# Optimization experiments

Measured on AMD Instinct MI355X. Metric: run time of the kernel, lower is better.

The kernel has to match this reference:

```python
import jax, jax.numpy as jnp
import numpy as np

S, D = 4096, 2048  # seq_len, embedding_space == qkv_dim


def setup_inputs() -> dict:
    key = jax.random.key(0)
    k1, k2, k3, k4, k5 = jax.random.split(key, 5)
    return {
        "input_embedding": jax.random.normal(k1, (S, D), dtype=jnp.float32),
        "query_embedding": jax.random.normal(k2, (S, D), dtype=jnp.float32),
        "Wq": jax.random.normal(k3, (D, D), dtype=jnp.float32) * 0.02,
        "Wk": jax.random.normal(k4, (D, D), dtype=jnp.float32) * 0.02,
        "Wv": jax.random.normal(k5, (D, D), dtype=jnp.float32) * 0.02,
        "include_mask": 0,  # False -> causal mask applied (module's inverted logic)
    }


def reference(input_embedding, query_embedding, Wq, Wk, Wv, include_mask):
    q = query_embedding @ Wq          # [S, D]
    k = input_embedding @ Wk          # [S, D]
    v = input_embedding @ Wv          # [S, D]
    scores = (q @ k.T) / 10.0         # [S, S]; module hardcodes /10, not sqrt(d)
    if not include_mask:
        # causal: -inf strictly above the diagonal (triu with offset 1)
        s = scores.shape[0]
        causal = jnp.tril(jnp.ones((s, s), dtype=bool))
        scores = jnp.where(causal, scores, -jnp.inf)
    probs = jax.nn.softmax(scores, axis=-1)
    return probs @ v                  # [S, D]
```

## Files before the change

kernel.cpp:

```cpp
#include <hip/hip_runtime.h>
#include <hip/hip_bf16.h>
#include <math.h>

typedef __bf16 bf16_t;
typedef __bf16 bf16x8 __attribute__((ext_vector_type(8)));
typedef float f32x4 __attribute__((ext_vector_type(4)));

enum { EP_BF16 = 0, EP_SCORES = 1, EP_F32 = 2, EP_F32A = 3 };

#define MEMFENCE asm volatile("" ::: "memory")
#define BARRIER() do { MEMFENCE; __builtin_amdgcn_s_barrier(); MEMFENCE; } while (0)

__device__ __forceinline__ void gload_lds16(const void* g, void* l) {
  __builtin_amdgcn_global_load_lds(
      (const __attribute__((address_space(1))) void*)g,
      (__attribute__((address_space(3))) void*)l, 16, 0, 0);
}

template <int N>
__device__ __forceinline__ void wait_vmcnt() {
  if constexpr (N == 0)       asm volatile("s_waitcnt vmcnt(0)" ::: "memory");
  else if constexpr (N == 6)  asm volatile("s_waitcnt vmcnt(6)" ::: "memory");
  else if constexpr (N == 8)  asm volatile("s_waitcnt vmcnt(8)" ::: "memory");
  else if constexpr (N == 12) asm volatile("s_waitcnt vmcnt(12)" ::: "memory");
  else if constexpr (N == 16) asm volatile("s_waitcnt vmcnt(16)" ::: "memory");
  else static_assert(N == 0, "unsupported vmcnt");
}

__device__ __forceinline__ int xcd_swz(int bid, int nwg) {
  const int q = nwg >> 3;
  return (bid & 7) * q + (bid >> 3);
}


template <int TM, bool STG, int WAITN>
__device__ __forceinline__ void do_tile(char* smem, int slot, int sslot, size_t stoff,
                                        const char* const* gbase, const int* lbase,
                                        const int* aoff, const int* boff,
                                        f32x4 (&acc)[TM][4]) {
  bf16x8 bfr[4], af[4];
  if constexpr (TM == 8) {
#pragma unroll
    for (int n = 0; n < 4; ++n) bfr[n] = *(const bf16x8*)(smem + slot + boff[n]);
#pragma unroll
    for (int m = 0; m < 4; ++m) af[m] = *(const bf16x8*)(smem + slot + aoff[m]);
    if constexpr (STG) {
      gload_lds16(gbase[0] + stoff, smem + sslot + lbase[0]);
      gload_lds16(gbase[1] + stoff, smem + sslot + lbase[1]);
    }
    BARRIER();
    asm volatile("s_waitcnt lgkmcnt(0)" ::: "memory");
    __builtin_amdgcn_sched_barrier(0);
    __builtin_amdgcn_s_setprio(1);
#pragma unroll
    for (int m = 0; m < 4; ++m)
#pragma unroll
      for (int n = 0; n < 4; ++n)
        acc[m][n] = __builtin_amdgcn_mfma_f32_16x16x32_bf16(af[m], bfr[n], acc[m][n], 0, 0, 0);
    __builtin_amdgcn_s_setprio(0);
    BARRIER();
#pragma unroll
    for (int m = 0; m < 4; ++m) af[m] = *(const bf16x8*)(smem + slot + aoff[4 + m]);
    if constexpr (STG) {
      gload_lds16(gbase[2] + stoff, smem + sslot + lbase[2]);
      gload_lds16(gbase[3] + stoff, smem + sslot + lbase[3]);
      wait_vmcnt<WAITN>();
    }
    BARRIER();
    asm volatile("s_waitcnt lgkmcnt(0)" ::: "memory");
    __builtin_amdgcn_sched_barrier(0);
    __builtin_amdgcn_s_setprio(1);
#pragma unroll
    for (int m = 0; m < 4; ++m)
#pragma unroll
      for (int n = 0; n < 4; ++n)
        acc[4 + m][n] = __builtin_amdgcn_mfma_f32_16x16x32_bf16(af[m], bfr[n], acc[4 + m][n], 0, 0, 0);
    __builtin_amdgcn_s_setprio(0);
    BARRIER();
  } else {
#pragma unroll
    for (int n = 0; n < 4; ++n) bfr[n] = *(const bf16x8*)(smem + slot + boff[n]);
#pragma unroll
    for (int m = 0; m < 4; ++m) af[m] = *(const bf16x8*)(smem + slot + aoff[m]);
    if constexpr (STG) {
      gload_lds16(gbase[0] + stoff, smem + sslot + lbase[0]);
      gload_lds16(gbase[1] + stoff, smem + sslot + lbase[1]);
      gload_lds16(gbase[2] + stoff, smem + sslot + lbase[2]);
      wait_vmcnt<WAITN>();
    }
    BARRIER();
    asm volatile("s_waitcnt lgkmcnt(0)" ::: "memory");
    __builtin_amdgcn_sched_barrier(0);
    __builtin_amdgcn_s_setprio(1);
#pragma unroll
    for (int m = 0; m < 4; ++m)
#pragma unroll
      for (int n = 0; n < 4; ++n)
        acc[m][n] = __builtin_amdgcn_mfma_f32_16x16x32_bf16(af[m], bfr[n], acc[m][n], 0, 0, 0);
    __builtin_amdgcn_s_setprio(0);
    BARRIER();
  }
}

template <int TM, int EPI, int NSLOT>
__device__ __forceinline__ void gemm_core(
    const bf16_t* __restrict__ A, const bf16_t* __restrict__ B,
    void* __restrict__ Cout, int Nout, int kstride, int klen,
    int row0, int col0, bool causal, float scale, char* smem)
{
  constexpr int BM = TM * 32;
  constexpr int LPT_A = BM / 128;
  constexpr int LPT = LPT_A + 2;
  constexpr int ABYTES = BM * 64;
  constexpr int SLOT = (BM + 256) * 64;
  constexpr int DEPTH = NSLOT - 1;
  constexpr int WAITN = (DEPTH - 1) * LPT;

  const int tid = threadIdx.x;
  const int w = tid >> 6, lane = tid & 63;
  const int wr = w >> 2, wc = w & 3;

  const int nt = klen >> 5;

  const char* gbase[LPT];
  int lbase[LPT];
  {
    const int sd = (tid & 3) ^ ((tid >> 3) & 3);
    const int rrow = tid >> 2;
#pragma unroll
    for (int r = 0; r < LPT; ++r) {
      const bool isA = (r < LPT_A);
      const int rr = isA ? r : (r - LPT_A);
      const int grow = (isA ? row0 : col0) + rr * 128 + rrow;
      const bf16_t* op = isA ? A : B;
      gbase[r] = (const char*)(op + (size_t)grow * kstride) + sd * 16;
      lbase[r] = (isA ? 0 : ABYTES) + rr * 8192 + w * 1024;
    }
  }

  const int fl = lane & 15;
  const int arow_off = fl * 64 + (((lane >> 4) ^ ((fl >> 1) & 3)) * 16);
  int aoff[TM], boff[4];
#pragma unroll
  for (int m = 0; m < TM; ++m) aoff[m] = (wr * (TM * 16) + m * 16) * 64 + arow_off;
#pragma unroll
  for (int n = 0; n < 4; ++n) boff[n] = ABYTES + (wc * 64 + n * 16) * 64 + arow_off;

  f32x4 acc[TM][4] = {};

  const int npro = nt < DEPTH ? nt : DEPTH;
  for (int t = 0; t < npro; ++t)
#pragma unroll
    for (int r = 0; r < LPT; ++r)
      gload_lds16(gbase[r] + (size_t)t * 64, smem + (t % NSLOT) * SLOT + lbase[r]);

  const int nmain = nt - DEPTH;
  if (nmain > 0) {
    wait_vmcnt<WAITN>();
    BARRIER();
    for (int t = 0; t < nmain; ++t)
      do_tile<TM, true, WAITN>(smem, (t % NSLOT) * SLOT, ((t + DEPTH) % NSLOT) * SLOT,
                               (size_t)(t + DEPTH) * 64, gbase, lbase, aoff, boff, acc);
  }

  wait_vmcnt<0>();
  BARRIER();
  for (int t = nmain > 0 ? nmain : 0; t < nt; ++t)
    do_tile<TM, false, 0>(smem, (t % NSLOT) * SLOT, 0, 0, gbase, lbase, aoff, boff, acc);

  const int cr = (lane >> 4) * 4;
  const int cc = lane & 15;
#pragma unroll
  for (int m = 0; m < TM; ++m) {
#pragma unroll
    for (int n = 0; n < 4; ++n) {
#pragma unroll
      for (int i = 0; i < 4; ++i) {
        const int r = row0 + wr * (TM * 16) + m * 16 + cr + i;
        const int c = col0 + wc * 64 + n * 16 + cc;
        float v = acc[m][n][i];
        if (EPI == EP_BF16) {
          ((bf16_t*)Cout)[(size_t)r * Nout + c] = (bf16_t)v;
        } else if (EPI == EP_SCORES) {
          v *= scale;
          if (causal && c > r) v = -INFINITY;
          ((float*)Cout)[(size_t)r * Nout + c] = v;
        } else if (EPI == EP_F32) {
          ((float*)Cout)[(size_t)r * Nout + c] = v;
        } else {
          atomicAdd((float*)Cout + (size_t)r * Nout + c, v);
        }
      }
    }
  }
}

__launch_bounds__(512, 2)
__global__ void qk_k(const bf16_t* __restrict__ qe16, const bf16_t* __restrict__ ie16,
                     const bf16_t* __restrict__ WqT, const bf16_t* __restrict__ WkT,
                     bf16_t* __restrict__ q16, bf16_t* __restrict__ k16) {
  extern __shared__ __align__(16) char smem[];
  int wg = xcd_swz(blockIdx.x, gridDim.x);
  const bf16_t *A, *B; bf16_t* C;
  if (wg < 128) { A = qe16; B = WqT; C = q16; }
  else          { A = ie16; B = WkT; C = k16; wg -= 128; }
  const int row0 = (wg >> 3) * 256, col0 = (wg & 7) * 256;
  gemm_core<8, EP_BF16, 4>(A, B, C, 2048, 2048, 2048, row0, col0, false, 1.f, smem);
}

__launch_bounds__(512, 2)
__global__ void vs_k(const bf16_t* __restrict__ WvT, const bf16_t* __restrict__ ie16,
                     const bf16_t* __restrict__ q16, const bf16_t* __restrict__ k16,
                     bf16_t* __restrict__ vT16, float* __restrict__ scores,
                     const int* __restrict__ maskflag) {
  extern __shared__ __align__(16) char smem[];
  const bool causal = maskflag[0] == 0;
  const int nsc = causal ? 136 : 256;
  const int bid = blockIdx.x;
  if (bid < nsc) {
    const int sid = xcd_swz(bid, nsc);
    int r, c;
    if (causal) {
      r = (int)((sqrtf(8.f * (float)sid + 1.f) - 1.f) * 0.5f);
      while ((r + 1) * (r + 2) / 2 <= sid) ++r;
      while (r * (r + 1) / 2 > sid) --r;
      c = sid - r * (r + 1) / 2;
    } else {
      r = sid >> 4; c = sid & 15;
    }
    gemm_core<8, EP_SCORES, 4>(q16, k16, scores, 4096, 2048, 2048,
                               r * 256, c * 256, causal, 0.1f, smem);
  } else {
    const int j = bid - nsc;
    gemm_core<4, EP_BF16, 6>(WvT, ie16, vT16, 4096, 2048, 2048,
                             (j >> 4) * 128, (j & 15) * 256, false, 1.f, smem);
  }
}

__launch_bounds__(512, 2)
__global__ void smv_k(const bf16_t* __restrict__ WvT, const bf16_t* __restrict__ ie16,
                      bf16_t* __restrict__ vT16,
                      const float* __restrict__ scores, bf16_t* __restrict__ probs,
                      const int* __restrict__ maskflag) {
  extern __shared__ __align__(16) char smem[];
  const bool causal = maskflag[0] == 0;
  const int nv = causal ? 136 : 256;
  const int vbase = causal ? 120 : 0;
  const int bid = blockIdx.x;
  if (bid < nv) {
    const int j = vbase + bid;
    gemm_core<4, EP_BF16, 6>(WvT, ie16, vT16, 4096, 2048, 2048,
                             (j >> 4) * 128, (j & 15) * 256, false, 1.f, smem);
    return;
  }
  const int p = bid - nv;
  if (p >= 2048) return;
  const int tid = threadIdx.x;
  const int h = tid >> 8;
  const int t = tid & 255;
  const int row = 2 * p + h;
  const int L = causal ? (row + 1) : 4096;
  const float* srow = scores + (size_t)row * 4096;
  float v[16];
  float m = -INFINITY;
#pragma unroll
  for (int j = 0; j < 16; ++j) {
    const int idx = t + j * 256;
    v[j] = (idx < L) ? srow[idx] : -INFINITY;
    m = fmaxf(m, v[j]);
  }
#pragma unroll
  for (int off = 32; off >= 1; off >>= 1) m = fmaxf(m, __shfl_xor(m, off));
  __shared__ float redm[8];
  __shared__ float reds[8];
  if ((tid & 63) == 0) redm[tid >> 6] = m;
  __syncthreads();
  m = fmaxf(fmaxf(redm[4 * h + 0], redm[4 * h + 1]),
            fmaxf(redm[4 * h + 2], redm[4 * h + 3]));
  float s = 0.f;
#pragma unroll
  for (int j = 0; j < 16; ++j) {
    v[j] = __expf(v[j] - m);
    s += v[j];
  }
#pragma unroll
  for (int off = 32; off >= 1; off >>= 1) s += __shfl_xor(s, off);
  if ((tid & 63) == 0) reds[tid >> 6] = s;
  __syncthreads();
  s = reds[4 * h + 0] + reds[4 * h + 1] + reds[4 * h + 2] + reds[4 * h + 3];
  const float inv = 1.f / s;
  bf16_t* prow = probs + (size_t)row * 4096;
#pragma unroll
  for (int j = 0; j < 16; ++j) prow[t + j * 256] = (bf16_t)(v[j] * inv);
}

__launch_bounds__(512, 2)
__global__ void pv_k(const bf16_t* __restrict__ probs, const bf16_t* __restrict__ vT16,
                     float* __restrict__ out, const int* __restrict__ maskflag) {
  extern __shared__ __align__(16) char smem[];
  const bool causal = maskflag[0] == 0;
  const int bid = blockIdx.x;
  if (causal) {
    if (bid >= 256) return;
    const int sid  = xcd_swz(bid, 256);
    const int half = sid & 1;
    const int pair = (sid >> 1) & 15;
    const int col  = sid >> 5;
    const int blo = pair, bhi = 31 - pair;
    const int Klo = 128 * (blo + 1);
    const int cut = 2112 - Klo;
    if (half == 0) {
      gemm_core<4, EP_F32, 6>(probs, vT16, out, 2048, 4096, Klo,
                              blo * 128, col * 256, false, 1.f, smem);
      __syncthreads();
      gemm_core<4, EP_F32A, 6>(probs, vT16, out, 2048, 4096, cut,
                               bhi * 128, col * 256, false, 1.f, smem);
    } else {
      gemm_core<4, EP_F32A, 6>(probs + cut, vT16 + cut, out, 2048, 4096, 2112,
                               bhi * 128, col * 256, false, 1.f, smem);
    }
  } else {
    if (bid >= 512) return;
    const int sid = xcd_swz(bid, 512);
    const int t = sid >> 1;
    const int band = t & 31, col = t >> 5;
    const int k0 = (sid & 1) ? 2048 : 0;
    gemm_core<4, EP_F32A, 6>(probs + k0, vT16 + k0, out, 2048, 4096, 2048,
                             band * 128, col * 256, false, 1.f, smem);
  }
}


__global__ void cvt_k(const float* __restrict__ qe, const float* __restrict__ ie,
                      bf16_t* __restrict__ qe16, bf16_t* __restrict__ ie16,
                      float* __restrict__ zout, long n) {
  const int y = blockIdx.y;
  long i = ((long)blockIdx.x * blockDim.x + threadIdx.x) * 8;
  const long stride = (long)gridDim.x * blockDim.x * 8;
  if (y == 2) {
    const float4 z = make_float4(0.f, 0.f, 0.f, 0.f);
    for (; i < n; i += stride) {
      *(float4*)(zout + i) = z;
      *(float4*)(zout + i + 4) = z;
    }
    return;
  }
  const float* x = y ? ie : qe;
  bf16_t* o = y ? ie16 : qe16;
  for (; i < n; i += stride) {
    const float4 a = *(const float4*)(x + i);
    const float4 b = *(const float4*)(x + i + 4);
    bf16x8 u;
    u[0] = (__bf16)a.x; u[1] = (__bf16)a.y; u[2] = (__bf16)a.z; u[3] = (__bf16)a.w;
    u[4] = (__bf16)b.x; u[5] = (__bf16)b.y; u[6] = (__bf16)b.z; u[7] = (__bf16)b.w;
    *(bf16x8*)(o + i) = u;
  }
}

__global__ void trans_k(const float* __restrict__ Wq, const float* __restrict__ Wk,
                        const float* __restrict__ Wv,
                        bf16_t* __restrict__ WqT, bf16_t* __restrict__ WkT,
                        bf16_t* __restrict__ WvT, int Dm) {
  const float* W = blockIdx.z == 0 ? Wq : (blockIdx.z == 1 ? Wk : Wv);
  bf16_t* WT = blockIdx.z == 0 ? WqT : (blockIdx.z == 1 ? WkT : WvT);
  __shared__ float tile[32][33];
  const int bx = blockIdx.x, by = blockIdx.y;
  const int tx = threadIdx.x & 31, ty = threadIdx.x >> 5;
#pragma unroll
  for (int r = ty; r < 32; r += 8)
    tile[r][tx] = W[(size_t)(by * 32 + r) * Dm + bx * 32 + tx];
  __syncthreads();
#pragma unroll
  for (int r = ty; r < 32; r += 8)
    WT[(size_t)(bx * 32 + r) * Dm + by * 32 + tx] = (bf16_t)tile[tx][r];
}

extern "C" void kernel_launch(void* const* d_in, const int* in_sizes, int n_in,
                              void* d_out, int out_size, void* d_ws, size_t ws_size,
                              hipStream_t stream) {
  const float* ie = (const float*)d_in[0];
  const float* qe = (const float*)d_in[1];
  const float* Wq = (const float*)d_in[2];
  const float* Wk = (const float*)d_in[3];
  const float* Wv = (const float*)d_in[4];
  const int* mask = (const int*)d_in[5];
  float* out = (float*)d_out;

  const int S = 4096, D = 2048;
  char* ws = (char*)d_ws;
  const size_t MB = 1u << 20;
  bf16_t* q16  = (bf16_t*)(ws + 0 * MB);
  bf16_t* k16  = (bf16_t*)(ws + 16 * MB);
  bf16_t* vT16 = (bf16_t*)(ws + 32 * MB);
  bf16_t* ie16 = (bf16_t*)(ws + 48 * MB);
  bf16_t* WvT  = (bf16_t*)(ws + 64 * MB);
  bf16_t* qe16 = (bf16_t*)(ws + 72 * MB);
  bf16_t* WqT  = (bf16_t*)(ws + 88 * MB);
  bf16_t* WkT  = (bf16_t*)(ws + 96 * MB);
  float*  scores = (float*)(ws + 72 * MB);
  bf16_t* probs  = (bf16_t*)(ws + 0 * MB);

  hipFuncSetAttribute(reinterpret_cast<const void*>(&qk_k),
                      hipFuncAttributeMaxDynamicSharedMemorySize, 131072);
  hipFuncSetAttribute(reinterpret_cast<const void*>(&vs_k),
                      hipFuncAttributeMaxDynamicSharedMemorySize, 147456);
  hipFuncSetAttribute(reinterpret_cast<const void*>(&smv_k),
                      hipFuncAttributeMaxDynamicSharedMemorySize, 147456);
  hipFuncSetAttribute(reinterpret_cast<const void*>(&pv_k),
                      hipFuncAttributeMaxDynamicSharedMemorySize, 147456);

  cvt_k<<<dim3(1024, 3), 256, 0, stream>>>(qe, ie, qe16, ie16, out, (long)S * D);
  trans_k<<<dim3(D / 32, D / 32, 3), 256, 0, stream>>>(Wq, Wk, Wv, WqT, WkT, WvT, D);

  qk_k<<<256, 512, 131072, stream>>>(qe16, ie16, WqT, WkT, q16, k16);

  vs_k<<<256, 512, 147456, stream>>>(WvT, ie16, q16, k16, vT16, scores, mask);

  smv_k<<<2304, 512, 147456, stream>>>(WvT, ie16, vT16, scores, probs, mask);

  pv_k<<<512, 512, 147456, stream>>>(probs, vT16, out, mask);
}
```

Before: 275.1 us.

## Halve barriers per k-step in GEMM main loops by merging half-tiles

For the 256-row tile variant, the two half-step phases (four barriers per k-tile) are merged into a single phase. It loads all eight A fragments at once, issues all four global-to-LDS loads together, and runs 32 MFMAs between one barrier pair. For the 128-row variant, two k-tiles are processed per iteration with one barrier pair, and prefetch depth drops from 5 to 4 tiles in 6 slots. The aim is to cut barrier and wait overhead and give the scheduler longer MFMA runs. The cost is more live fragment registers and shallower prefetch lookahead for the 128-row path.

```diff
diff --git a/kernel.cpp b/kernel.cpp
--- a/kernel.cpp
+++ b/kernel.cpp
@@ -19,11 +19,9 @@
 
 template <int N>
 __device__ __forceinline__ void wait_vmcnt() {
-  if constexpr (N == 0)       asm volatile("s_waitcnt vmcnt(0)" ::: "memory");
-  else if constexpr (N == 6)  asm volatile("s_waitcnt vmcnt(6)" ::: "memory");
-  else if constexpr (N == 8)  asm volatile("s_waitcnt vmcnt(8)" ::: "memory");
-  else if constexpr (N == 12) asm volatile("s_waitcnt vmcnt(12)" ::: "memory");
-  else if constexpr (N == 16) asm volatile("s_waitcnt vmcnt(16)" ::: "memory");
+  if constexpr (N == 0)      asm volatile("s_waitcnt vmcnt(0)" ::: "memory");
+  else if constexpr (N == 6) asm volatile("s_waitcnt vmcnt(6)" ::: "memory");
+  else if constexpr (N == 8) asm volatile("s_waitcnt vmcnt(8)" ::: "memory");
   else static_assert(N == 0, "unsupported vmcnt");
 }
 
@@ -33,76 +31,71 @@
 }
 
 
-template <int TM, bool STG, int WAITN>
-__device__ __forceinline__ void do_tile(char* smem, int slot, int sslot, size_t stoff,
-                                        const char* const* gbase, const int* lbase,
-                                        const int* aoff, const int* boff,
-                                        f32x4 (&acc)[TM][4]) {
-  bf16x8 bfr[4], af[4];
-  if constexpr (TM == 8) {
-#pragma unroll
-    for (int n = 0; n < 4; ++n) bfr[n] = *(const bf16x8*)(smem + slot + boff[n]);
-#pragma unroll
-    for (int m = 0; m < 4; ++m) af[m] = *(const bf16x8*)(smem + slot + aoff[m]);
-    if constexpr (STG) {
-      gload_lds16(gbase[0] + stoff, smem + sslot + lbase[0]);
-      gload_lds16(gbase[1] + stoff, smem + sslot + lbase[1]);
-    }
-    BARRIER();
-    asm volatile("s_waitcnt lgkmcnt(0)" ::: "memory");
-    __builtin_amdgcn_sched_barrier(0);
-    __builtin_amdgcn_s_setprio(1);
-#pragma unroll
-    for (int m = 0; m < 4; ++m)
-#pragma unroll
-      for (int n = 0; n < 4; ++n)
-        acc[m][n] = __builtin_amdgcn_mfma_f32_16x16x32_bf16(af[m], bfr[n], acc[m][n], 0, 0, 0);
-    __builtin_amdgcn_s_setprio(0);
-    BARRIER();
-#pragma unroll
-    for (int m = 0; m < 4; ++m) af[m] = *(const bf16x8*)(smem + slot + aoff[4 + m]);
-    if constexpr (STG) {
-      gload_lds16(gbase[2] + stoff, smem + sslot + lbase[2]);
-      gload_lds16(gbase[3] + stoff, smem + sslot + lbase[3]);
-      wait_vmcnt<WAITN>();
-    }
-    BARRIER();
-    asm volatile("s_waitcnt lgkmcnt(0)" ::: "memory");
-    __builtin_amdgcn_sched_barrier(0);
-    __builtin_amdgcn_s_setprio(1);
-#pragma unroll
-    for (int m = 0; m < 4; ++m)
-#pragma unroll
-      for (int n = 0; n < 4; ++n)
-        acc[4 + m][n] = __builtin_amdgcn_mfma_f32_16x16x32_bf16(af[m], bfr[n], acc[4 + m][n], 0, 0, 0);
-    __builtin_amdgcn_s_setprio(0);
-    BARRIER();
-  } else {
-#pragma unroll
-    for (int n = 0; n < 4; ++n) bfr[n] = *(const bf16x8*)(smem + slot + boff[n]);
-#pragma unroll
-    for (int m = 0; m < 4; ++m) af[m] = *(const bf16x8*)(smem + slot + aoff[m]);
-    if constexpr (STG) {
-      gload_lds16(gbase[0] + stoff, smem + sslot + lbase[0]);
-      gload_lds16(gbase[1] + stoff, smem + sslot + lbase[1]);
-      gload_lds16(gbase[2] + stoff, smem + sslot + lbase[2]);
-      wait_vmcnt<WAITN>();
-    }
-    BARRIER();
-    asm volatile("s_waitcnt lgkmcnt(0)" ::: "memory");
-    __builtin_amdgcn_sched_barrier(0);
-    __builtin_amdgcn_s_setprio(1);
-#pragma unroll
-    for (int m = 0; m < 4; ++m)
-#pragma unroll
-      for (int n = 0; n < 4; ++n)
-        acc[m][n] = __builtin_amdgcn_mfma_f32_16x16x32_bf16(af[m], bfr[n], acc[m][n], 0, 0, 0);
-    __builtin_amdgcn_s_setprio(0);
-    BARRIER();
-  }
-}
-
-template <int TM, int EPI, int NSLOT>
+template <bool STG, int WAITN>
+__device__ __forceinline__ void do_tile8(char* smem, int slot, int sslot, size_t stoff,
+                                         const char* const* gbase, const int* lbase,
+                                         const int* aoff, const int* boff,
+                                         f32x4 (&acc)[8][4]) {
+  bf16x8 bfr[4], af[8];
+#pragma unroll
+  for (int n = 0; n < 4; ++n) bfr[n] = *(const bf16x8*)(smem + slot + boff[n]);
+#pragma unroll
+  for (int m = 0; m < 8; ++m) af[m] = *(const bf16x8*)(smem + slot + aoff[m]);
+  if constexpr (STG) {
+#pragma unroll
+    for (int r = 0; r < 4; ++r) gload_lds16(gbase[r] + stoff, smem + sslot + lbase[r]);
+    wait_vmcnt<WAITN>();
+  }
+  BARRIER();
+  __builtin_amdgcn_s_setprio(1);
+#pragma unroll
+  for (int m = 0; m < 8; ++m)
+#pragma unroll
+    for (int n = 0; n < 4; ++n)
+      acc[m][n] = __builtin_amdgcn_mfma_f32_16x16x32_bf16(af[m], bfr[n], acc[m][n], 0, 0, 0);
+  __builtin_amdgcn_s_setprio(0);
+  BARRIER();
+}
+
+template <bool STG, int WAITN>
+__device__ __forceinline__ void do_tile4x2(char* smem, int slot0, int slot1,
+                                           int ss0, int ss1, size_t st0, size_t st1,
+                                           const char* const* gbase, const int* lbase,
+                                           const int* aoff, const int* boff,
+                                           f32x4 (&acc)[4][4]) {
+  bf16x8 b0[4], a0[4], b1[4], a1[4];
+#pragma unroll
+  for (int n = 0; n < 4; ++n) b0[n] = *(const bf16x8*)(smem + slot0 + boff[n]);
+#pragma unroll
+  for (int m = 0; m < 4; ++m) a0[m] = *(const bf16x8*)(smem + slot0 + aoff[m]);
+#pragma unroll
+  for (int n = 0; n < 4; ++n) b1[n] = *(const bf16x8*)(smem + slot1 + boff[n]);
+#pragma unroll
+  for (int m = 0; m < 4; ++m) a1[m] = *(const bf16x8*)(smem + slot1 + aoff[m]);
+  if constexpr (STG) {
+#pragma unroll
+    for (int r = 0; r < 3; ++r) gload_lds16(gbase[r] + st0, smem + ss0 + lbase[r]);
+#pragma unroll
+    for (int r = 0; r < 3; ++r) gload_lds16(gbase[r] + st1, smem + ss1 + lbase[r]);
+    wait_vmcnt<WAITN>();
+  }
+  BARRIER();
+  __builtin_amdgcn_s_setprio(1);
+#pragma unroll
+  for (int m = 0; m < 4; ++m)
+#pragma unroll
+    for (int n = 0; n < 4; ++n)
+      acc[m][n] = __builtin_amdgcn_mfma_f32_16x16x32_bf16(a0[m], b0[n], acc[m][n], 0, 0, 0);
+#pragma unroll
+  for (int m = 0; m < 4; ++m)
+#pragma unroll
+    for (int n = 0; n < 4; ++n)
+      acc[m][n] = __builtin_amdgcn_mfma_f32_16x16x32_bf16(a1[m], b1[n], acc[m][n], 0, 0, 0);
+  __builtin_amdgcn_s_setprio(0);
+  BARRIER();
+}
+
+template <int TM, int EPI>
 __device__ __forceinline__ void gemm_core(
     const bf16_t* __restrict__ A, const bf16_t* __restrict__ B,
     void* __restrict__ Cout, int Nout, int kstride, int klen,
@@ -113,8 +106,9 @@
   constexpr int LPT = LPT_A + 2;
   constexpr int ABYTES = BM * 64;
   constexpr int SLOT = (BM + 256) * 64;
-  constexpr int DEPTH = NSLOT - 1;
-  constexpr int WAITN = (DEPTH - 1) * LPT;
+  constexpr int NSLOT = (TM == 8) ? 4 : 6;
+  constexpr int DEPTH = (TM == 8) ? 3 : 4;
+  constexpr int WAITN = (TM == 8) ? 8 : 6;
 
   const int tid = threadIdx.x;
   const int w = tid >> 6, lane = tid & 63;
@@ -158,15 +152,30 @@
   if (nmain > 0) {
     wait_vmcnt<WAITN>();
     BARRIER();
-    for (int t = 0; t < nmain; ++t)
-      do_tile<TM, true, WAITN>(smem, (t % NSLOT) * SLOT, ((t + DEPTH) % NSLOT) * SLOT,
-                               (size_t)(t + DEPTH) * 64, gbase, lbase, aoff, boff, acc);
+    if constexpr (TM == 8) {
+      for (int t = 0; t < nmain; ++t)
+        do_tile8<true, WAITN>(smem, (t % NSLOT) * SLOT, ((t + DEPTH) % NSLOT) * SLOT,
+                              (size_t)(t + DEPTH) * 64, gbase, lbase, aoff, boff, acc);
+    } else {
+      for (int t = 0; t + 2 <= nmain; t += 2)
+        do_tile4x2<true, WAITN>(smem, (t % NSLOT) * SLOT, ((t + 1) % NSLOT) * SLOT,
+                                ((t + DEPTH) % NSLOT) * SLOT, ((t + DEPTH + 1) % NSLOT) * SLOT,
+                                (size_t)(t + DEPTH) * 64, (size_t)(t + DEPTH + 1) * 64,
+                                gbase, lbase, aoff, boff, acc);
+    }
   }
 
   wait_vmcnt<0>();
   BARRIER();
-  for (int t = nmain > 0 ? nmain : 0; t < nt; ++t)
-    do_tile<TM, false, 0>(smem, (t % NSLOT) * SLOT, 0, 0, gbase, lbase, aoff, boff, acc);
+  const int t0 = nmain > 0 ? nmain : 0;
+  if constexpr (TM == 8) {
+    for (int t = t0; t < nt; ++t)
+      do_tile8<false, 0>(smem, (t % NSLOT) * SLOT, 0, 0, gbase, lbase, aoff, boff, acc);
+  } else {
+    for (int t = t0; t < nt; t += 2)
+      do_tile4x2<false, 0>(smem, (t % NSLOT) * SLOT, ((t + 1) % NSLOT) * SLOT,
+                           0, 0, 0, 0, gbase, lbase, aoff, boff, acc);
+  }
 
   const int cr = (lane >> 4) * 4;
   const int cc = lane & 15;
@@ -205,7 +214,7 @@
   if (wg < 128) { A = qe16; B = WqT; C = q16; }
   else          { A = ie16; B = WkT; C = k16; wg -= 128; }
   const int row0 = (wg >> 3) * 256, col0 = (wg & 7) * 256;
-  gemm_core<8, EP_BF16, 4>(A, B, C, 2048, 2048, 2048, row0, col0, false, 1.f, smem);
+  gemm_core<8, EP_BF16>(A, B, C, 2048, 2048, 2048, row0, col0, false, 1.f, smem);
 }
 
 __launch_bounds__(512, 2)
@@ -228,12 +237,12 @@
     } else {
       r = sid >> 4; c = sid & 15;
     }
-    gemm_core<8, EP_SCORES, 4>(q16, k16, scores, 4096, 2048, 2048,
-                               r * 256, c * 256, causal, 0.1f, smem);
+    gemm_core<8, EP_SCORES>(q16, k16, scores, 4096, 2048, 2048,
+                            r * 256, c * 256, causal, 0.1f, smem);
   } else {
     const int j = bid - nsc;
-    gemm_core<4, EP_BF16, 6>(WvT, ie16, vT16, 4096, 2048, 2048,
-                             (j >> 4) * 128, (j & 15) * 256, false, 1.f, smem);
+    gemm_core<4, EP_BF16>(WvT, ie16, vT16, 4096, 2048, 2048,
+                          (j >> 4) * 128, (j & 15) * 256, false, 1.f, smem);
   }
 }
 
@@ -249,8 +258,8 @@
   const int bid = blockIdx.x;
   if (bid < nv) {
     const int j = vbase + bid;
-    gemm_core<4, EP_BF16, 6>(WvT, ie16, vT16, 4096, 2048, 2048,
-                             (j >> 4) * 128, (j & 15) * 256, false, 1.f, smem);
+    gemm_core<4, EP_BF16>(WvT, ie16, vT16, 4096, 2048, 2048,
+                          (j >> 4) * 128, (j & 15) * 256, false, 1.f, smem);
     return;
   }
   const int p = bid - nv;
@@ -310,14 +319,14 @@
     const int Klo = 128 * (blo + 1);
     const int cut = 2112 - Klo;
     if (half == 0) {
-      gemm_core<4, EP_F32, 6>(probs, vT16, out, 2048, 4096, Klo,
-                              blo * 128, col * 256, false, 1.f, smem);
+      gemm_core<4, EP_F32>(probs, vT16, out, 2048, 4096, Klo,
+                           blo * 128, col * 256, false, 1.f, smem);
       __syncthreads();
-      gemm_core<4, EP_F32A, 6>(probs, vT16, out, 2048, 4096, cut,
-                               bhi * 128, col * 256, false, 1.f, smem);
+      gemm_core<4, EP_F32A>(probs, vT16, out, 2048, 4096, cut,
+                            bhi * 128, col * 256, false, 1.f, smem);
     } else {
-      gemm_core<4, EP_F32A, 6>(probs + cut, vT16 + cut, out, 2048, 4096, 2112,
-                               bhi * 128, col * 256, false, 1.f, smem);
+      gemm_core<4, EP_F32A>(probs + cut, vT16 + cut, out, 2048, 4096, 2112,
+                            bhi * 128, col * 256, false, 1.f, smem);
     }
   } else {
     if (bid >= 512) return;
@@ -325,8 +334,8 @@
     const int t = sid >> 1;
     const int band = t & 31, col = t >> 5;
     const int k0 = (sid & 1) ? 2048 : 0;
-    gemm_core<4, EP_F32A, 6>(probs + k0, vT16 + k0, out, 2048, 4096, 2048,
-                             band * 128, col * 256, false, 1.f, smem);
+    gemm_core<4, EP_F32A>(probs + k0, vT16 + k0, out, 2048, 4096, 2048,
+                          band * 128, col * 256, false, 1.f, smem);
   }
 }
 
```

New measurement: 281.9 us. 1.02x slower.

## Rebalance causal PV split-K with fixed-point integer atomics and larger tiles

Applied to the files above, without the earlier changes.

Reworks the probs@V kernel to use 256-row tiles (TM=8, 4-stage) and an even split-K partition across 32 causal work units per column, pairing low and high row bands into equal-length K windows. Partial sums are accumulated with integer atomics in 2^24 fixed point, and a new pass converts the output back to float. This is meant to balance work across blocks and make accumulation deterministic, at the cost of an extra full-output pass and possible precision or overflow trouble for large values.

```diff
diff --git a/kernel.cpp b/kernel.cpp
--- a/kernel.cpp
+++ b/kernel.cpp
@@ -6,7 +6,7 @@
 typedef __bf16 bf16x8 __attribute__((ext_vector_type(8)));
 typedef float f32x4 __attribute__((ext_vector_type(4)));
 
-enum { EP_BF16 = 0, EP_SCORES = 1, EP_F32 = 2, EP_F32A = 3 };
+enum { EP_BF16 = 0, EP_SCORES = 1, EP_F32 = 2, EP_F32A = 3, EP_I32A = 4 };
 
 #define MEMFENCE asm volatile("" ::: "memory")
 #define BARRIER() do { MEMFENCE; __builtin_amdgcn_s_barrier(); MEMFENCE; } while (0)
@@ -187,8 +187,11 @@
           ((float*)Cout)[(size_t)r * Nout + c] = v;
         } else if (EPI == EP_F32) {
           ((float*)Cout)[(size_t)r * Nout + c] = v;
+        } else if (EPI == EP_F32A) {
+          atomicAdd((float*)Cout + (size_t)r * Nout + c, v);
         } else {
-          atomicAdd((float*)Cout + (size_t)r * Nout + c, v);
+          atomicAdd((int*)Cout + (size_t)r * Nout + c,
+                    __float2int_rn(v * 16777216.0f));
         }
       }
     }
@@ -296,37 +299,52 @@
 
 __launch_bounds__(512, 2)
 __global__ void pv_k(const bf16_t* __restrict__ probs, const bf16_t* __restrict__ vT16,
-                     float* __restrict__ out, const int* __restrict__ maskflag) {
+                     int* __restrict__ iout, const int* __restrict__ maskflag) {
   extern __shared__ __align__(16) char smem[];
   const bool causal = maskflag[0] == 0;
   const int bid = blockIdx.x;
+  const int col = bid & 7;
   if (causal) {
-    if (bid >= 256) return;
-    const int sid  = xcd_swz(bid, 256);
-    const int half = sid & 1;
-    const int pair = (sid >> 1) & 15;
-    const int col  = sid >> 5;
-    const int blo = pair, bhi = 31 - pair;
-    const int Klo = 128 * (blo + 1);
-    const int cut = 2112 - Klo;
-    if (half == 0) {
-      gemm_core<4, EP_F32, 6>(probs, vT16, out, 2048, 4096, Klo,
-                              blo * 128, col * 256, false, 1.f, smem);
+    const int idx = bid >> 3;
+    if (idx >= 32) return;
+    const int p = idx >> 2;
+    const int wnd = idx & 3;
+    const int blo = p, bhi = 15 - p;
+    const int Klo = 8 * (p + 1);
+    const int Khi = 128 - 8 * p;
+    const int w0 = 34 * wnd, w1 = w0 + 34;
+    const int l0 = w0, l1 = min(w1, Klo);
+    if (l0 < l1) {
+      gemm_core<8, EP_I32A, 4>(probs + l0 * 32, vT16 + l0 * 32, iout, 2048, 4096,
+                               (l1 - l0) * 32, blo * 256, col * 256, false, 1.f, smem);
       __syncthreads();
-      gemm_core<4, EP_F32A, 6>(probs, vT16, out, 2048, 4096, cut,
-                               bhi * 128, col * 256, false, 1.f, smem);
-    } else {
-      gemm_core<4, EP_F32A, 6>(probs + cut, vT16 + cut, out, 2048, 4096, 2112,
-                               bhi * 128, col * 256, false, 1.f, smem);
+    }
+    const int h0 = max(w0 - Klo, 0), h1 = min(w1 - Klo, Khi);
+    if (h0 < h1) {
+      gemm_core<8, EP_I32A, 4>(probs + h0 * 32, vT16 + h0 * 32, iout, 2048, 4096,
+                               (h1 - h0) * 32, bhi * 256, col * 256, false, 1.f, smem);
     }
   } else {
-    if (bid >= 512) return;
-    const int sid = xcd_swz(bid, 512);
-    const int t = sid >> 1;
-    const int band = t & 31, col = t >> 5;
-    const int k0 = (sid & 1) ? 2048 : 0;
-    gemm_core<4, EP_F32A, 6>(probs + k0, vT16 + k0, out, 2048, 4096, 2048,
-                             band * 128, col * 256, false, 1.f, smem);
+    const int q = bid >> 3;
+    if (q >= 64) return;
+    const int band = q >> 2;
+    const int k0 = (q & 3) * 1024;
+    gemm_core<8, EP_I32A, 4>(probs + k0, vT16 + k0, iout, 2048, 4096, 1024,
+                             band * 256, col * 256, false, 1.f, smem);
+  }
+}
+
+__global__ void cvtout_k(float* __restrict__ out, long n) {
+  long i = ((long)blockIdx.x * blockDim.x + threadIdx.x) * 4;
+  const long stride = (long)gridDim.x * blockDim.x * 4;
+  for (; i < n; i += stride) {
+    int4 v = *(const int4*)((const int*)out + i);
+    float4 f;
+    f.x = (float)v.x * (1.0f / 16777216.0f);
+    f.y = (float)v.y * (1.0f / 16777216.0f);
+    f.z = (float)v.z * (1.0f / 16777216.0f);
+    f.w = (float)v.w * (1.0f / 16777216.0f);
+    *(float4*)(out + i) = f;
   }
 }
 
@@ -407,7 +425,7 @@
   hipFuncSetAttribute(reinterpret_cast<const void*>(&smv_k),
                       hipFuncAttributeMaxDynamicSharedMemorySize, 147456);
   hipFuncSetAttribute(reinterpret_cast<const void*>(&pv_k),
-                      hipFuncAttributeMaxDynamicSharedMemorySize, 147456);
+                      hipFuncAttributeMaxDynamicSharedMemorySize, 131072);
 
   cvt_k<<<dim3(1024, 3), 256, 0, stream>>>(qe, ie, qe16, ie16, out, (long)S * D);
   trans_k<<<dim3(D / 32, D / 32, 3), 256, 0, stream>>>(Wq, Wk, Wv, WqT, WkT, WvT, D);
@@ -418,5 +436,7 @@
 
   smv_k<<<2304, 512, 147456, stream>>>(WvT, ie16, vT16, scores, probs, mask);
 
-  pv_k<<<512, 512, 147456, stream>>>(probs, vT16, out, mask);
-}
+  pv_k<<<512, 512, 131072, stream>>>(probs, vT16, (int*)out, mask);
+
+  cvtout_k<<<2048, 256, 0, stream>>>(out, (long)S * D);
+}
```

Result: slower. 304.6 us (+10.7%).

## Use larger V-projection tiles and split-K the last tile row with integer atomics

Applied to the files above, without the earlier changes.

The V projection now uses 256x256 tiles (TM=8) in both vs_k and smv3_k, so fewer and larger blocks are needed. In the causal case the final 256-row band of V^T is split along K into four pieces. The pieces are accumulated with fixed-point int32 atomics into a zeroed buffer, and a new small kernel converts that buffer to bf16. The goal is better balance for the leftover V work that runs alongside softmax. The cost is an extra kernel launch, an extra buffer zeroing pass, and fixed-point quantisation at a 2^24 scale, which could overflow for large values.

```diff
diff --git a/kernel.cpp b/kernel.cpp
--- a/kernel.cpp
+++ b/kernel.cpp
@@ -6,7 +6,7 @@
 typedef __bf16 bf16x8 __attribute__((ext_vector_type(8)));
 typedef float f32x4 __attribute__((ext_vector_type(4)));
 
-enum { EP_BF16 = 0, EP_SCORES = 1, EP_F32 = 2, EP_F32A = 3 };
+enum { EP_BF16 = 0, EP_SCORES = 1, EP_F32 = 2, EP_F32A = 3, EP_I32A = 4 };
 
 #define MEMFENCE asm volatile("" ::: "memory")
 #define BARRIER() do { MEMFENCE; __builtin_amdgcn_s_barrier(); MEMFENCE; } while (0)
@@ -23,7 +23,6 @@
   else if constexpr (N == 6)  asm volatile("s_waitcnt vmcnt(6)" ::: "memory");
   else if constexpr (N == 8)  asm volatile("s_waitcnt vmcnt(8)" ::: "memory");
   else if constexpr (N == 12) asm volatile("s_waitcnt vmcnt(12)" ::: "memory");
-  else if constexpr (N == 16) asm volatile("s_waitcnt vmcnt(16)" ::: "memory");
   else static_assert(N == 0, "unsupported vmcnt");
 }
 
@@ -187,8 +186,11 @@
           ((float*)Cout)[(size_t)r * Nout + c] = v;
         } else if (EPI == EP_F32) {
           ((float*)Cout)[(size_t)r * Nout + c] = v;
+        } else if (EPI == EP_F32A) {
+          atomicAdd((float*)Cout + (size_t)r * Nout + c, v);
         } else {
-          atomicAdd((float*)Cout + (size_t)r * Nout + c, v);
+          atomicAdd((int*)Cout + (size_t)r * Nout + c,
+                    __float2int_rn(v * 16777216.0f));
         }
       }
     }
@@ -232,25 +234,34 @@
                                r * 256, c * 256, causal, 0.1f, smem);
   } else {
     const int j = bid - nsc;
-    gemm_core<4, EP_BF16, 6>(WvT, ie16, vT16, 4096, 2048, 2048,
-                             (j >> 4) * 128, (j & 15) * 256, false, 1.f, smem);
+    if (j >= 120) return;
+    gemm_core<8, EP_BF16, 4>(WvT, ie16, vT16, 4096, 2048, 2048,
+                             (j >> 4) * 256, (j & 15) * 256, false, 1.f, smem);
   }
 }
 
 __launch_bounds__(512, 2)
-__global__ void smv_k(const bf16_t* __restrict__ WvT, const bf16_t* __restrict__ ie16,
-                      bf16_t* __restrict__ vT16,
-                      const float* __restrict__ scores, bf16_t* __restrict__ probs,
-                      const int* __restrict__ maskflag) {
+__global__ void smv3_k(const bf16_t* __restrict__ WvT, const bf16_t* __restrict__ ie16,
+                       bf16_t* __restrict__ vT16, int* __restrict__ vT32i,
+                       const float* __restrict__ scores, bf16_t* __restrict__ probs,
+                       const int* __restrict__ maskflag) {
   extern __shared__ __align__(16) char smem[];
   const bool causal = maskflag[0] == 0;
-  const int nv = causal ? 136 : 256;
-  const int vbase = causal ? 120 : 0;
+  const int nv = causal ? 32 : 128;
   const int bid = blockIdx.x;
   if (bid < nv) {
-    const int j = vbase + bid;
-    gemm_core<4, EP_BF16, 6>(WvT, ie16, vT16, 4096, 2048, 2048,
-                             (j >> 4) * 128, (j & 15) * 256, false, 1.f, smem);
+    if (causal) {
+      const int ov = bid & 7;
+      const int piece = bid >> 3;
+      const bf16_t* A = WvT + (size_t)1792 * 2048 + piece * 512;
+      const bf16_t* B = ie16 + (size_t)(2048 + ov * 256) * 2048 + piece * 512;
+      gemm_core<8, EP_I32A, 4>(A, B, vT32i + ov * 65536, 256, 2048, 512,
+                               0, 0, false, 1.f, smem);
+    } else {
+      const int j = bid;
+      gemm_core<8, EP_BF16, 4>(WvT, ie16, vT16, 4096, 2048, 2048,
+                               (j >> 4) * 256, (j & 15) * 256, false, 1.f, smem);
+    }
     return;
   }
   const int p = bid - nv;
@@ -292,6 +303,28 @@
   bf16_t* prow = probs + (size_t)row * 4096;
 #pragma unroll
   for (int j = 0; j < 16; ++j) prow[t + j * 256] = (bf16_t)(v[j] * inv);
+}
+
+__global__ void cvt8_k(const int* __restrict__ vT32i, bf16_t* __restrict__ vT16,
+                       const int* __restrict__ maskflag) {
+  if (maskflag[0] != 0) return;
+  const long i = ((long)blockIdx.x * blockDim.x + threadIdx.x) * 8;
+  if (i >= 8L * 65536) return;
+  const int tile = (int)(i >> 16);
+  const int within = (int)(i & 65535);
+  const int r = within >> 8, c = within & 255;
+  const int4 a = *(const int4*)(vT32i + i);
+  const int4 b = *(const int4*)(vT32i + i + 4);
+  bf16x8 o;
+  o[0] = (__bf16)((float)a.x * (1.0f / 16777216.0f));
+  o[1] = (__bf16)((float)a.y * (1.0f / 16777216.0f));
+  o[2] = (__bf16)((float)a.z * (1.0f / 16777216.0f));
+  o[3] = (__bf16)((float)a.w * (1.0f / 16777216.0f));
+  o[4] = (__bf16)((float)b.x * (1.0f / 16777216.0f));
+  o[5] = (__bf16)((float)b.y * (1.0f / 16777216.0f));
+  o[6] = (__bf16)((float)b.z * (1.0f / 16777216.0f));
+  o[7] = (__bf16)((float)b.w * (1.0f / 16777216.0f));
+  *(bf16x8*)(vT16 + (size_t)(1792 + r) * 4096 + (8 + tile) * 256 + c) = o;
 }
 
 __launch_bounds__(512, 2)
@@ -333,15 +366,17 @@
 
 __global__ void cvt_k(const float* __restrict__ qe, const float* __restrict__ ie,
                       bf16_t* __restrict__ qe16, bf16_t* __restrict__ ie16,
-                      float* __restrict__ zout, long n) {
+                      float* __restrict__ zout, float* __restrict__ zv, long n) {
   const int y = blockIdx.y;
   long i = ((long)blockIdx.x * blockDim.x + threadIdx.x) * 8;
   const long stride = (long)gridDim.x * blockDim.x * 8;
-  if (y == 2) {
-    const float4 z = make_float4(0.f, 0.f, 0.f, 0.f);
-    for (; i < n; i += stride) {
-      *(float4*)(zout + i) = z;
-      *(float4*)(zout + i + 4) = z;
+  if (y >= 2) {
+    float* z = (y == 2) ? zout : zv;
+    const long nz = (y == 2) ? n : 8L * 65536;
+    const float4 zero4 = make_float4(0.f, 0.f, 0.f, 0.f);
+    for (; i < nz; i += stride) {
+      *(float4*)(z + i) = zero4;
+      *(float4*)(z + i + 4) = zero4;
     }
     return;
   }
@@ -399,24 +434,27 @@
   bf16_t* WkT  = (bf16_t*)(ws + 96 * MB);
   float*  scores = (float*)(ws + 72 * MB);
   bf16_t* probs  = (bf16_t*)(ws + 0 * MB);
+  float*  vT32   = (float*)(ws + 136 * MB);
 
   hipFuncSetAttribute(reinterpret_cast<const void*>(&qk_k),
                       hipFuncAttributeMaxDynamicSharedMemorySize, 131072);
   hipFuncSetAttribute(reinterpret_cast<const void*>(&vs_k),
-                      hipFuncAttributeMaxDynamicSharedMemorySize, 147456);
-  hipFuncSetAttribute(reinterpret_cast<const void*>(&smv_k),
-                      hipFuncAttributeMaxDynamicSharedMemorySize, 147456);
+                      hipFuncAttributeMaxDynamicSharedMemorySize, 131072);
+  hipFuncSetAttribute(reinterpret_cast<const void*>(&smv3_k),
+                      hipFuncAttributeMaxDynamicSharedMemorySize, 131072);
   hipFuncSetAttribute(reinterpret_cast<const void*>(&pv_k),
                       hipFuncAttributeMaxDynamicSharedMemorySize, 147456);
 
-  cvt_k<<<dim3(1024, 3), 256, 0, stream>>>(qe, ie, qe16, ie16, out, (long)S * D);
+  cvt_k<<<dim3(1024, 4), 256, 0, stream>>>(qe, ie, qe16, ie16, out, vT32, (long)S * D);
   trans_k<<<dim3(D / 32, D / 32, 3), 256, 0, stream>>>(Wq, Wk, Wv, WqT, WkT, WvT, D);
 
   qk_k<<<256, 512, 131072, stream>>>(qe16, ie16, WqT, WkT, q16, k16);
 
-  vs_k<<<256, 512, 147456, stream>>>(WvT, ie16, q16, k16, vT16, scores, mask);
-
-  smv_k<<<2304, 512, 147456, stream>>>(WvT, ie16, vT16, scores, probs, mask);
+  vs_k<<<256, 512, 131072, stream>>>(WvT, ie16, q16, k16, vT16, scores, mask);
+
+  smv3_k<<<2176, 512, 131072, stream>>>(WvT, ie16, vT16, (int*)vT32, scores, probs, mask);
+
+  cvt8_k<<<256, 256, 0, stream>>>((const int*)vT32, vT16, mask);
 
   pv_k<<<512, 512, 147456, stream>>>(probs, vT16, out, mask);
 }
```

After: 268.5 us (median of 2 runs). 1.02x faster.
